# Performance work log

Hardware: AMD Instinct MI355X
Metric: run time of the kernel (lower is better)

## Reference

```python
import jax, jax.numpy as jnp
import numpy as np

NUM_WIRES = 18
N_LAYERS = 3
BATCH = 128
DIM = 2 ** NUM_WIRES


def setup_inputs() -> dict:
    key = jax.random.key(0)
    k1, k2, k3, k4, k5 = jax.random.split(key, 5)
    sr = jax.random.normal(k1, (BATCH, DIM), jnp.float32)
    si = jax.random.normal(k2, (BATCH, DIM), jnp.float32)
    norm = jnp.sqrt(jnp.sum(sr * sr + si * si, axis=1, keepdims=True))
    sr = sr / norm
    si = si / norm
    params = jax.random.normal(k3, (N_LAYERS, NUM_WIRES, 3), jnp.float32)
    head_w = jax.random.normal(k4, (1, NUM_WIRES), jnp.float32) * 0.1
    head_b = jax.random.normal(k5, (1,), jnp.float32) * 0.1
    return {"state_real": sr, "state_imag": si, "params": params,
            "head_w": head_w, "head_b": head_b}


def _gate_u(p):
    """Fused 2x2 unitary U = RZ(p2) @ RY(p1) @ RX(p0) (RX applied first)."""
    x, y, z = p[0], p[1], p[2]
    cx = jnp.cos(x / 2).astype(jnp.complex64)
    sx = jnp.sin(x / 2).astype(jnp.complex64)
    cy = jnp.cos(y / 2).astype(jnp.complex64)
    sy = jnp.sin(y / 2).astype(jnp.complex64)
    zero = jnp.zeros((), jnp.complex64)
    RX = jnp.stack([jnp.stack([cx, -1j * sx]), jnp.stack([-1j * sx, cx])])
    RY = jnp.stack([jnp.stack([cy, -sy]), jnp.stack([sy, cy])])
    ez = jnp.exp(-0.5j * z.astype(jnp.complex64))  # e^{-i z/2}
    RZ = jnp.stack([jnp.stack([ez, zero]), jnp.stack([zero, jnp.conj(ez)])])
    return RZ @ RY @ RX


def _apply_1q(state, U, w):
    # wire 0 = most significant bit (PennyLane default.qubit convention)
    b = state.shape[0]
    A = 2 ** w
    B = DIM // (2 * A)
    s = state.reshape(b, A, 2, B)
    s = jnp.einsum('ij,bajc->baic', U, s)
    return s.reshape(b, DIM)


def _apply_cz(state, w):
    b = state.shape[0]
    A = 2 ** w
    B = DIM // (4 * A)
    s = state.reshape(b, A, 2, 2, B)
    s = s.at[:, :, 1, 1, :].multiply(-1.0)
    return s.reshape(b, DIM)


def reference(state_real, state_imag, params, head_w, head_b):
    state = (state_real + 1j * state_imag).astype(jnp.complex64)
    for l in range(N_LAYERS):
        for w in range(NUM_WIRES):
            state = _apply_1q(state, _gate_u(params[l, w]), w)
        for w in range(NUM_WIRES - 1):
            state = _apply_cz(state, w)
    probs = state.real ** 2 + state.imag ** 2  # (B, DIM)
    feats = []
    for w in range(NUM_WIRES):
        A = 2 ** w
        B = DIM // (2 * A)
        p = probs.reshape(-1, A, 2, B).sum(axis=(1, 3))  # (batch, 2)
        feats.append(p[:, 0] - p[:, 1])  # <Z_w>
    feats = jnp.stack(feats, axis=1)  # (batch, num_wires)
    return (feats @ head_w.T + head_b)[:, 0]
```

## Files before the change

kernel.cpp:

```cpp
#include <hip/hip_runtime.h>

#define DBITS 18

typedef float v2f __attribute__((ext_vector_type(2)));

__device__ __forceinline__ int physx(int j){ return j ^ ((j>>4)&15) ^ ((j>>8)&15) ^ ((j>>12)&1); }

template<int b0,int b1,int b2,int b3>
__device__ __forceinline__ int dep4(int c){
  return ((c&1)<<b0) | (((c>>1)&1)<<b1) | (((c>>2)&1)<<b2) | (((c>>3)&1)<<b3);
}
template<int b0,int b1,int b2,int b3>
__device__ __forceinline__ int pdep4(int c){
  const int d = dep4<b0,b1,b2,b3>(c);
  return d ^ ((d>>4)&15) ^ ((d>>8)&15) ^ ((d>>12)&1);
}

__device__ __forceinline__ unsigned pack_bf2(v2f v){
  unsigned ur = __float_as_uint(v.x), ui = __float_as_uint(v.y);
  ur = (ur + 0x7FFFu + ((ur >> 16) & 1u)) >> 16;
  ui = (ui + 0x7FFFu + ((ui >> 16) & 1u)) & 0xFFFF0000u;
  return ur | ui;
}
__device__ __forceinline__ v2f unpack_bf2(unsigned u){
  v2f v; v.x = __uint_as_float(u << 16); v.y = __uint_as_float(u & 0xFFFF0000u); return v;
}

__device__ __forceinline__ v2f pk_mul(v2f x, v2f s){
  v2f r; asm("v_pk_mul_f32 %0, %1, %2" : "=v"(r) : "v"(x), "v"(s)); return r;
}
__device__ __forceinline__ v2f pk_mul_neg(v2f x, v2f s){
  v2f r; asm("v_pk_mul_f32 %0, %1, %2 neg_lo:[1,0] neg_hi:[1,0]" : "=v"(r) : "v"(x), "v"(s)); return r;
}
__device__ __forceinline__ v2f pk_fma(v2f x, v2f s, v2f a){
  v2f r; asm("v_pk_fma_f32 %0, %1, %2, %3" : "=v"(r) : "v"(x), "v"(s), "v"(a)); return r;
}
__device__ __forceinline__ v2f pk_fma_swlo(v2f x, v2f s, v2f a){
  v2f r; asm("v_pk_fma_f32 %0, %1, %2, %3 op_sel:[1,0,0] op_sel_hi:[0,1,1] neg_lo:[1,0,0]"
             : "=v"(r) : "v"(x), "v"(s), "v"(a)); return r;
}
__device__ __forceinline__ v2f pk_fma_swhi(v2f x, v2f s, v2f a){
  v2f r; asm("v_pk_fma_f32 %0, %1, %2, %3 op_sel:[1,0,0] op_sel_hi:[0,1,1] neg_hi:[1,0,0]"
             : "=v"(r) : "v"(x), "v"(s), "v"(a)); return r;
}

template<int S>
__device__ __forceinline__ void gate_pk(v2f a[16], const float* __restrict__ g){
  const v2f Ar = {g[0],g[0]}, Ai = {g[1],g[1]}, Br = {g[2],g[2]}, Bi = {g[3],g[3]};
  #pragma unroll
  for (int h = 0; h < 8; ++h){
    const int c0 = ((h & ~(S-1)) << 1) | (h & (S-1));
    const int c1 = c0 | S;
    const v2f X0 = a[c0], X1 = a[c1];
    v2f y0 = pk_mul(X0, Ar);
    y0 = pk_fma_swlo(X0, Ai, y0);
    y0 = pk_fma(X1, Br, y0);
    y0 = pk_fma_swlo(X1, Bi, y0);
    v2f y1 = pk_mul_neg(X0, Br);
    y1 = pk_fma_swlo(X0, Bi, y1);
    y1 = pk_fma(X1, Ar, y1);
    y1 = pk_fma_swhi(X1, Ai, y1);
    a[c0] = y0; a[c1] = y1;
  }
}

template<int CTRL>
__device__ __forceinline__ float dppf(float v){
  return __int_as_float(__builtin_amdgcn_update_dpp(0, __float_as_int(v), CTRL, 0xF, 0xF, true));
}
template<int CTRL>
__device__ __forceinline__ void gate_lane_pk(v2f a[16], const float* __restrict__ g, float s){
  const float uei = s*g[1], uor = s*g[2];
  const v2f UER = {g[0],g[0]}, UEI = {uei,uei}, UOR = {uor,uor}, UOI = {g[3],g[3]};
  #pragma unroll
  for (int c = 0; c < 16; ++c){
    const v2f X = a[c];
    v2f P; P.x = dppf<CTRL>(X.x); P.y = dppf<CTRL>(X.y);
    v2f y = pk_mul(X, UER);
    y = pk_fma_swlo(X, UEI, y);
    y = pk_fma(P, UOR, y);
    y = pk_fma_swlo(P, UOI, y);
    a[c] = y;
  }
}

__device__ __forceinline__ const float* gp(const float* __restrict__ gates, int L, int ggbit){
  return gates + (L*18 + (17 - ggbit))*4;
}
__device__ __forceinline__ void sgn(v2f& v, unsigned gg){
  const unsigned sb = (unsigned)(__popc(gg & (gg >> 1)) & 1) << 31;
  v.x = __uint_as_float(__float_as_uint(v.x) ^ sb);
  v.y = __uint_as_float(__float_as_uint(v.y) ^ sb);
}

template<int PASS>
__global__ __launch_bounds__(512, 4)
void qpass(const float* __restrict__ sr, const float* __restrict__ si,
           unsigned* __restrict__ st, const float* __restrict__ gates,
           const float* __restrict__ head_w, float* __restrict__ partials,
           int batch0)
{
  __shared__ v2f lds[8192];
  const int t = threadIdx.x;
  const int f  = (int)blockIdx.x & 31;
  const int bl = (int)blockIdx.x >> 5;
  const int bg = batch0 + bl;
  const unsigned stBase = ((unsigned)bl) << DBITS;
  const size_t  inBase  = ((size_t)bg) << DBITS;
  const float s1 = (t & 1) ? -1.f : 1.f;
  const float s2 = (t & 2) ? -1.f : 1.f;

  v2f a[16];

  if (PASS == 1){
    {
      const size_t base = inBase + ((size_t)f << 13) + (size_t)t;
      #pragma unroll
      for (int c = 0; c < 16; ++c){
        const size_t g = base + ((size_t)c << 9);
        a[c].x = sr[g]; a[c].y = si[g];
      }
      gate_pk<1>(a, gp(gates,0,9));
      gate_pk<2>(a, gp(gates,0,10));
      gate_pk<4>(a, gp(gates,0,11));
      gate_pk<8>(a, gp(gates,0,12));
      gate_lane_pk<0xB1>(a, gp(gates,0,0), s1);
      gate_lane_pk<0x4E>(a, gp(gates,0,1), s2);
      const int pj = physx(t);
      #pragma unroll
      for (int c = 0; c < 16; ++c) lds[pj ^ pdep4<9,10,11,12>(c)] = a[c];
    }
    __syncthreads();
    {
      const int jb = ((t&1)<<6)|(((t>>1)&1)<<7)|(((t>>2)&1)<<0)|(((t>>3)&1)<<1)|((t>>4)<<8);
      const int pj = physx(jb);
      #pragma unroll
      for (int c = 0; c < 16; ++c) a[c] = lds[pj ^ pdep4<2,3,4,5>(c)];
      gate_pk<1>(a, gp(gates,0,2));
      gate_pk<2>(a, gp(gates,0,3));
      gate_pk<4>(a, gp(gates,0,4));
      gate_pk<8>(a, gp(gates,0,5));
      gate_lane_pk<0xB1>(a, gp(gates,0,6), s1);
      gate_lane_pk<0x4E>(a, gp(gates,0,7), s2);
      #pragma unroll
      for (int c = 0; c < 16; ++c) lds[pj ^ pdep4<2,3,4,5>(c)] = a[c];
    }
    __syncthreads();
    {
      const int jb = (t&63)|(((t>>6)&1)<<6)|(((t>>7)&1)<<7)|(((t>>8)&1)<<12);
      const int pj = physx(jb);
      #pragma unroll
      for (int c = 0; c < 16; ++c) a[c] = lds[pj ^ pdep4<8,9,10,11>(c)];
      gate_pk<1>(a, gp(gates,0,8));
      const unsigned gb = (unsigned)(jb | (f << 13)) + stBase;
      #pragma unroll
      for (int c = 0; c < 16; ++c) st[gb + (unsigned)dep4<8,9,10,11>(c)] = pack_bf2(a[c]);
    }
  }
  else if (PASS == 2){
    {
      const unsigned gb = stBase + (unsigned)((t&255) | (((t>>8)&1)<<13) | (f<<8));
      #pragma unroll
      for (int c = 0; c < 16; ++c) a[c] = unpack_bf2(st[gb + ((unsigned)c<<14)]);
      gate_pk<1>(a, gp(gates,0,14));
      gate_pk<2>(a, gp(gates,0,15));
      gate_pk<4>(a, gp(gates,0,16));
      gate_pk<8>(a, gp(gates,0,17));
      const int pj = physx(t);
      #pragma unroll
      for (int c = 0; c < 16; ++c) lds[pj ^ pdep4<9,10,11,12>(c)] = a[c];
    }
    __syncthreads();
    {
      const int jb = ((t&1)<<10)|(((t>>1)&1)<<11)|(((t>>2)&1)<<0)|(((t>>3)&1)<<1)
                   | (((t>>4)&1)<<5)|(((t>>5)&1)<<6)|(((t>>6)&1)<<7)|(((t>>7)&1)<<9)|(((t>>8)&1)<<12);
      const int pj = physx(jb);
      #pragma unroll
      for (int c = 0; c < 16; ++c) a[c] = lds[pj ^ pdep4<8,2,3,4>(c)];
      gate_pk<1>(a, gp(gates,0,13));
      const unsigned gsb = (unsigned)((jb&255) | ((jb>>8)<<13) | (f<<8));
      #pragma unroll
      for (int c = 0; c < 16; ++c)
        sgn(a[c], gsb | (unsigned)(((c&1)<<13)|(((c>>1)&1)<<2)|(((c>>2)&1)<<3)|(((c>>3)&1)<<4)));
      gate_pk<1>(a, gp(gates,1,13));
      gate_pk<2>(a, gp(gates,1,2));
      gate_pk<4>(a, gp(gates,1,3));
      gate_pk<8>(a, gp(gates,1,4));
      gate_lane_pk<0xB1>(a, gp(gates,1,15), s1);
      gate_lane_pk<0x4E>(a, gp(gates,1,16), s2);
      #pragma unroll
      for (int c = 0; c < 16; ++c) lds[pj ^ pdep4<8,2,3,4>(c)] = a[c];
    }
    __syncthreads();
    {
      const int jb = (t&63)|(((t>>6)&1)<<8)|(((t>>7)&1)<<10)|(((t>>8)&1)<<11);
      const int pj = physx(jb);
      #pragma unroll
      for (int c = 0; c < 16; ++c) a[c] = lds[pj ^ pdep4<6,7,9,12>(c)];
      gate_pk<1>(a, gp(gates,1,6));
      gate_pk<2>(a, gp(gates,1,7));
      gate_pk<4>(a, gp(gates,1,14));
      gate_pk<8>(a, gp(gates,1,17));
      gate_lane_pk<0xB1>(a, gp(gates,1,0), s1);
      gate_lane_pk<0x4E>(a, gp(gates,1,1), s2);
      #pragma unroll
      for (int c = 0; c < 16; ++c){
        const int j = jb | dep4<6,7,9,12>(c);
        st[stBase + (unsigned)((j&255) | ((j>>8)<<13) | (f<<8))] = pack_bf2(a[c]);
      }
    }
  }
  else if (PASS == 3){
    const unsigned fp3 = (unsigned)(((f&3)<<6) | (((f>>2)&7)<<14));
    {
      const unsigned gb = stBase + (unsigned)((t&63) | (((t>>6)&7)<<8)) + fp3;
      #pragma unroll
      for (int c = 0; c < 16; ++c)
        a[c] = unpack_bf2(st[gb + (unsigned)(((c&7)<<11) | (((c>>3)&1)<<17))]);
      gate_pk<1>(a, gp(gates,1,11));
      gate_pk<2>(a, gp(gates,1,12));
      const int pj = physx(t);
      #pragma unroll
      for (int c = 0; c < 16; ++c) lds[pj ^ pdep4<9,10,11,12>(c)] = a[c];
    }
    __syncthreads();
    {
      const int jb = ((t&1)<<11)|(((t>>1)&1)<<12)|(((t>>2)&1)<<1)|(((t>>3)&1)<<2)
                   | (((t>>4)&1)<<0)|(((t>>5)&1)<<3)|(((t>>6)&1)<<4)|(((t>>7)&1)<<9)|(((t>>8)&1)<<10);
      const int pj = physx(jb);
      #pragma unroll
      for (int c = 0; c < 16; ++c) a[c] = lds[pj ^ pdep4<5,6,7,8>(c)];
      gate_pk<1>(a, gp(gates,1,5));
      gate_pk<2>(a, gp(gates,1,8));
      gate_pk<4>(a, gp(gates,1,9));
      gate_pk<8>(a, gp(gates,1,10));
      const unsigned gsb = (unsigned)((jb&63) | (((jb>>6)&63)<<8) | (((jb>>12)&1)<<17)) | fp3;
      #pragma unroll
      for (int c = 0; c < 16; ++c)
        sgn(a[c], gsb | (unsigned)(((c&1)<<5)|(((c>>1)&1)<<8)|(((c>>2)&1)<<9)|(((c>>3)&1)<<10)));
      gate_pk<1>(a, gp(gates,2,5));
      gate_pk<2>(a, gp(gates,2,8));
      gate_pk<4>(a, gp(gates,2,9));
      gate_pk<8>(a, gp(gates,2,10));
      gate_lane_pk<0xB1>(a, gp(gates,2,13), s1);
      gate_lane_pk<0x4E>(a, gp(gates,2,17), s2);
      #pragma unroll
      for (int c = 0; c < 16; ++c) lds[pj ^ pdep4<5,6,7,8>(c)] = a[c];
    }
    __syncthreads();
    {
      const int jb = (t&63)|(((t>>6)&1)<<6)|(((t>>7)&1)<<7)|(((t>>8)&1)<<12);
      const int pj = physx(jb);
      #pragma unroll
      for (int c = 0; c < 16; ++c) a[c] = lds[pj ^ pdep4<9,10,8,11>(c)];
      gate_pk<1>(a, gp(gates,2,11));
      gate_pk<2>(a, gp(gates,2,12));
      gate_lane_pk<0xB1>(a, gp(gates,2,0), s1);
      gate_lane_pk<0x4E>(a, gp(gates,2,1), s2);
      #pragma unroll
      for (int c = 0; c < 16; ++c){
        const int j = jb | dep4<9,10,8,11>(c);
        st[stBase + ((unsigned)((j&63) | (((j>>6)&63)<<8) | (((j>>12)&1)<<17)) | fp3)] = pack_bf2(a[c]);
      }
    }
  }
  else {
    const unsigned fp4 = (unsigned)(((f&15)<<10) | (((f>>4)&1)<<17));
    {
      const unsigned gb = stBase + (unsigned)t + fp4;
      #pragma unroll
      for (int c = 0; c < 16; ++c)
        a[c] = unpack_bf2(st[gb + (unsigned)(((c&1)<<9) | (((c>>1)&7)<<14))]);
      gate_pk<2>(a, gp(gates,2,14));
      gate_pk<4>(a, gp(gates,2,15));
      gate_pk<8>(a, gp(gates,2,16));
      const int pj = physx(t);
      #pragma unroll
      for (int c = 0; c < 16; ++c) lds[pj ^ pdep4<9,10,11,12>(c)] = a[c];
    }
    __syncthreads();
    {
      const int jb = ((t&1)<<7)|(((t>>1)&1)<<5)|(((t>>2)&1)<<0)|(((t>>3)&1)<<10)
                   | (((t>>4)&1)<<1)|(((t>>5)&1)<<8)|(((t>>6)&1)<<9)|(((t>>7)&1)<<11)|(((t>>8)&1)<<12);
      const int pj = physx(jb);
      #pragma unroll
      for (int c = 0; c < 16; ++c) a[c] = lds[pj ^ pdep4<2,3,4,6>(c)];
      gate_pk<1>(a, gp(gates,2,2));
      gate_pk<2>(a, gp(gates,2,3));
      gate_pk<4>(a, gp(gates,2,4));
      gate_pk<8>(a, gp(gates,2,6));
      gate_lane_pk<0xB1>(a, gp(gates,2,7), s1);
      const unsigned gg0 = (unsigned)((jb&1023) | (((jb>>10)&7)<<14)) | fp4;
      float cb = 0.f;
      #pragma unroll
      for (int k = 0; k < 18; ++k){
        const float hw = head_w[17-k];
        cb += ((gg0 >> k) & 1) ? -hw : hw;
      }
      const float d0 = -2.f*head_w[15], d1 = -2.f*head_w[14];
      const float d2 = -2.f*head_w[13], d3 = -2.f*head_w[11];
      float acc = 0.f;
      #pragma unroll
      for (int c = 0; c < 16; ++c){
        float coef = cb;
        if (c & 1) coef += d0;
        if (c & 2) coef += d1;
        if (c & 4) coef += d2;
        if (c & 8) coef += d3;
        acc += coef * (a[c].x*a[c].x + a[c].y*a[c].y);
      }
      __syncthreads();
      #pragma unroll
      for (int off = 32; off; off >>= 1) acc += __shfl_down(acc, off);
      float* red = reinterpret_cast<float*>(lds);
      if ((t & 63) == 0) red[t >> 6] = acc;
      __syncthreads();
      if (t == 0){
        float s = 0.f;
        #pragma unroll
        for (int i = 0; i < 8; ++i) s += red[i];
        partials[bg * 32 + f] = s;
      }
    }
  }
}

__global__ void qprep(const float* __restrict__ params, float* __restrict__ gates){
  const int tid = threadIdx.x;
  if (tid < 54){
    const float xx = params[tid*3+0]*0.5f, yy = params[tid*3+1]*0.5f, zz = params[tid*3+2]*0.5f;
    float sx,cx,sy,cy,sz,cz;
    sincosf(xx,&sx,&cx); sincosf(yy,&sy,&cy); sincosf(zz,&sz,&cz);
    float* g = gates + tid*4;
    g[0] =  cz*cy*cx + sz*sy*sx;
    g[1] =  cz*sy*sx - sz*cy*cx;
    g[2] = -cz*sy*cx - sz*cy*sx;
    g[3] =  sz*sy*cx - cz*cy*sx;
  }
}

__global__ void qfinal(const float* __restrict__ partials, const float* __restrict__ head_b,
                       float* __restrict__ out, int B){
  const int b = threadIdx.x + blockIdx.x * blockDim.x;
  if (b < B){
    float s = head_b[0];
    #pragma unroll
    for (int i = 0; i < 32; ++i) s += partials[b*32 + i];
    out[b] = s;
  }
}

extern "C" void kernel_launch(void* const* d_in, const int* in_sizes, int n_in,
                              void* d_out, int out_size, void* d_ws, size_t ws_size,
                              hipStream_t stream){
  const float* sr     = (const float*)d_in[0];
  const float* si     = (const float*)d_in[1];
  const float* params = (const float*)d_in[2];
  const float* head_w = (const float*)d_in[3];
  const float* head_b = (const float*)d_in[4];
  float* out = (float*)d_out;
  const int B = in_sizes[0] >> DBITS;

  float*    gates    = (float*)d_ws;
  float*    partials = (float*)((char*)d_ws + 4096);
  unsigned* st       = (unsigned*)((char*)d_ws + 24576);

  size_t stBytes = ws_size > 24576 ? ws_size - 24576 : 0;
  int maxChunk = (int)(stBytes / ((size_t)(1 << DBITS) * 4));
  if (maxChunk > B) maxChunk = B;
  if (maxChunk < 1) maxChunk = 1;

  qprep<<<dim3(1), dim3(64), 0, stream>>>(params, gates);

  for (int b0 = 0; b0 < B; b0 += maxChunk){
    const int c = (B - b0 < maxChunk) ? (B - b0) : maxChunk;
    dim3 grid(c * 32), blk(512);
    qpass<1><<<grid, blk, 0, stream>>>(sr, si, st, gates, head_w, partials, b0);
    qpass<2><<<grid, blk, 0, stream>>>(sr, si, st, gates, head_w, partials, b0);
    qpass<3><<<grid, blk, 0, stream>>>(sr, si, st, gates, head_w, partials, b0);
    qpass<4><<<grid, blk, 0, stream>>>(sr, si, st, gates, head_w, partials, b0);
  }
  qfinal<<<dim3(1), dim3(128), 0, stream>>>(partials, head_b, out, B);
}
```

Baseline: 395.3 us.

## Repartition passes to 1024-thread blocks with 8 amplitudes per thread and XCD-aware block remap

Restructures all four state-vector passes so each 1024-thread block holds an 8192-amplitude tile, with 8 amplitudes per thread instead of 16. The wire-to-pass assignment, LDS swizzle and global access patterns are redesigned: the first pass uses float4 loads, later passes fuse more gates and CZ sign flips per pass, and the last pass no longer needs an LDS exchange. A block-index remap spreads consecutive logical tiles across the 8 XCDs for L2 locality. This aims to cut register pressure and raise occupancy and memory coalescing, at the cost of bigger blocks, new swizzle logic and more warps per reduction.

After: 401.3 us. Within noise of the previous version (+1.5%).

```diff
diff --git a/kernel.cpp b/kernel.cpp
--- a/kernel.cpp
+++ b/kernel.cpp
@@ -4,17 +4,16 @@
 
 typedef float v2f __attribute__((ext_vector_type(2)));
 
-__device__ __forceinline__ int physx(int j){ return j ^ ((j>>4)&15) ^ ((j>>8)&15) ^ ((j>>12)&1); }
-
-template<int b0,int b1,int b2,int b3>
-__device__ __forceinline__ int dep4(int c){
-  return ((c&1)<<b0) | (((c>>1)&1)<<b1) | (((c>>2)&1)<<b2) | (((c>>3)&1)<<b3);
-}
-template<int b0,int b1,int b2,int b3>
-__device__ __forceinline__ int pdep4(int c){
-  const int d = dep4<b0,b1,b2,b3>(c);
-  return d ^ ((d>>4)&15) ^ ((d>>8)&15) ^ ((d>>12)&1);
-}
+__device__ __forceinline__ constexpr int physb(int j){
+  return j ^ (((j>>4)&1)<<1) ^ (((j>>5)&1)<<2) ^ (((j>>6)&1)<<3) ^ (((j>>6)&1)<<0)
+           ^ (((j>>8)&1)<<2) ^ (((j>>9)&1)<<3);
+}
+template<int b0,int b1,int b2>
+__device__ __forceinline__ int dep3(int c){
+  return ((c&1)<<b0) | (((c>>1)&1)<<b1) | (((c>>2)&1)<<b2);
+}
+template<int b0,int b1,int b2>
+__device__ __forceinline__ int pb3(int c){ return physb(dep3<b0,b1,b2>(c)); }
 
 __device__ __forceinline__ unsigned pack_bf2(v2f v){
   unsigned ur = __float_as_uint(v.x), ui = __float_as_uint(v.y);
@@ -45,10 +44,10 @@
 }
 
 template<int S>
-__device__ __forceinline__ void gate_pk(v2f a[16], const float* __restrict__ g){
+__device__ __forceinline__ void gate_pk8(v2f a[8], const float* __restrict__ g){
   const v2f Ar = {g[0],g[0]}, Ai = {g[1],g[1]}, Br = {g[2],g[2]}, Bi = {g[3],g[3]};
   #pragma unroll
-  for (int h = 0; h < 8; ++h){
+  for (int h = 0; h < 4; ++h){
     const int c0 = ((h & ~(S-1)) << 1) | (h & (S-1));
     const int c1 = c0 | S;
     const v2f X0 = a[c0], X1 = a[c1];
@@ -69,11 +68,11 @@
   return __int_as_float(__builtin_amdgcn_update_dpp(0, __float_as_int(v), CTRL, 0xF, 0xF, true));
 }
 template<int CTRL>
-__device__ __forceinline__ void gate_lane_pk(v2f a[16], const float* __restrict__ g, float s){
+__device__ __forceinline__ void gate_lane8(v2f a[8], const float* __restrict__ g, float s){
   const float uei = s*g[1], uor = s*g[2];
   const v2f UER = {g[0],g[0]}, UEI = {uei,uei}, UOR = {uor,uor}, UOI = {g[3],g[3]};
   #pragma unroll
-  for (int c = 0; c < 16; ++c){
+  for (int c = 0; c < 8; ++c){
     const v2f X = a[c];
     v2f P; P.x = dppf<CTRL>(X.x); P.y = dppf<CTRL>(X.y);
     v2f y = pk_mul(X, UER);
@@ -94,7 +93,7 @@
 }
 
 template<int PASS>
-__global__ __launch_bounds__(512, 4)
+__global__ __launch_bounds__(1024, 8)
 void qpass(const float* __restrict__ sr, const float* __restrict__ si,
            unsigned* __restrict__ st, const float* __restrict__ gates,
            const float* __restrict__ head_w, float* __restrict__ partials,
@@ -102,214 +101,203 @@
 {
   __shared__ v2f lds[8192];
   const int t = threadIdx.x;
-  const int f  = (int)blockIdx.x & 31;
-  const int bl = (int)blockIdx.x >> 5;
+
+  const int nwg = (int)gridDim.x;
+  const int p = (int)blockIdx.x;
+  const int q = nwg >> 3, r = nwg & 7, x = p & 7, m = p >> 3;
+  const int logical = (x < r ? x*(q+1) : r*(q+1) + (x-r)*q) + m;
+  const int f  = logical & 31;
+  const int bl = logical >> 5;
   const int bg = batch0 + bl;
   const unsigned stBase = ((unsigned)bl) << DBITS;
   const size_t  inBase  = ((size_t)bg) << DBITS;
   const float s1 = (t & 1) ? -1.f : 1.f;
   const float s2 = (t & 2) ? -1.f : 1.f;
 
-  v2f a[16];
+  v2f a[8];
 
   if (PASS == 1){
     {
-      const size_t base = inBase + ((size_t)f << 13) + (size_t)t;
-      #pragma unroll
-      for (int c = 0; c < 16; ++c){
-        const size_t g = base + ((size_t)c << 9);
-        a[c].x = sr[g]; a[c].y = si[g];
-      }
-      gate_pk<1>(a, gp(gates,0,9));
-      gate_pk<2>(a, gp(gates,0,10));
-      gate_pk<4>(a, gp(gates,0,11));
-      gate_pk<8>(a, gp(gates,0,12));
-      gate_lane_pk<0xB1>(a, gp(gates,0,0), s1);
-      gate_lane_pk<0x4E>(a, gp(gates,0,1), s2);
-      const int pj = physx(t);
-      #pragma unroll
-      for (int c = 0; c < 16; ++c) lds[pj ^ pdep4<9,10,11,12>(c)] = a[c];
-    }
-    __syncthreads();
-    {
-      const int jb = ((t&1)<<6)|(((t>>1)&1)<<7)|(((t>>2)&1)<<0)|(((t>>3)&1)<<1)|((t>>4)<<8);
-      const int pj = physx(jb);
-      #pragma unroll
-      for (int c = 0; c < 16; ++c) a[c] = lds[pj ^ pdep4<2,3,4,5>(c)];
-      gate_pk<1>(a, gp(gates,0,2));
-      gate_pk<2>(a, gp(gates,0,3));
-      gate_pk<4>(a, gp(gates,0,4));
-      gate_pk<8>(a, gp(gates,0,5));
-      gate_lane_pk<0xB1>(a, gp(gates,0,6), s1);
-      gate_lane_pk<0x4E>(a, gp(gates,0,7), s2);
-      #pragma unroll
-      for (int c = 0; c < 16; ++c) lds[pj ^ pdep4<2,3,4,5>(c)] = a[c];
-    }
-    __syncthreads();
-    {
-      const int jb = (t&63)|(((t>>6)&1)<<6)|(((t>>7)&1)<<7)|(((t>>8)&1)<<12);
-      const int pj = physx(jb);
-      #pragma unroll
-      for (int c = 0; c < 16; ++c) a[c] = lds[pj ^ pdep4<8,9,10,11>(c)];
-      gate_pk<1>(a, gp(gates,0,8));
-      const unsigned gb = (unsigned)(jb | (f << 13)) + stBase;
-      #pragma unroll
-      for (int c = 0; c < 16; ++c) st[gb + (unsigned)dep4<8,9,10,11>(c)] = pack_bf2(a[c]);
+      const int jb = ((t&1)<<3) | (((t>>1)&1)<<4) | ((t>>2)<<5);
+      const size_t base = inBase + ((size_t)f << 13) + (size_t)jb;
+      const float4 r0 = *(const float4*)(sr+base);
+      const float4 r1 = *(const float4*)(sr+base+4);
+      const float4 i0 = *(const float4*)(si+base);
+      const float4 i1 = *(const float4*)(si+base+4);
+      a[0] = {r0.x,i0.x}; a[1] = {r0.y,i0.y}; a[2] = {r0.z,i0.z}; a[3] = {r0.w,i0.w};
+      a[4] = {r1.x,i1.x}; a[5] = {r1.y,i1.y}; a[6] = {r1.z,i1.z}; a[7] = {r1.w,i1.w};
+      gate_pk8<1>(a, gp(gates,0,0));
+      gate_pk8<2>(a, gp(gates,0,1));
+      gate_pk8<4>(a, gp(gates,0,2));
+      gate_lane8<0xB1>(a, gp(gates,0,3), s1);
+      gate_lane8<0x4E>(a, gp(gates,0,4), s2);
+      const int pj = physb(jb);
+      #pragma unroll
+      for (int c = 0; c < 8; ++c) lds[pj ^ pb3<0,1,2>(c)] = a[c];
+    }
+    __syncthreads();
+    {
+      const int jb = ((t&1)<<8)|(((t>>1)&1)<<9)|(((t>>2)&1)<<0)|(((t>>3)&1)<<1)
+                   | (((t>>4)&1)<<2)|(((t>>5)&1)<<3)|(((t>>6)&1)<<4)
+                   | (((t>>7)&1)<<10)|(((t>>8)&1)<<11)|(((t>>9)&1)<<12);
+      const int pj = physb(jb);
+      #pragma unroll
+      for (int c = 0; c < 8; ++c) a[c] = lds[pj ^ pb3<5,6,7>(c)];
+      gate_pk8<1>(a, gp(gates,0,5));
+      gate_pk8<2>(a, gp(gates,0,6));
+      gate_pk8<4>(a, gp(gates,0,7));
+      gate_lane8<0xB1>(a, gp(gates,0,8), s1);
+      gate_lane8<0x4E>(a, gp(gates,0,9), s2);
+      #pragma unroll
+      for (int c = 0; c < 8; ++c) lds[pj ^ pb3<5,6,7>(c)] = a[c];
+    }
+    __syncthreads();
+    {
+      const int pj = physb(t);
+      #pragma unroll
+      for (int c = 0; c < 8; ++c) a[c] = lds[pj ^ pb3<10,11,12>(c)];
+      gate_pk8<1>(a, gp(gates,0,10));
+      gate_pk8<2>(a, gp(gates,0,11));
+      gate_pk8<4>(a, gp(gates,0,12));
+      const unsigned gb = stBase + (unsigned)((f<<13) | t);
+      #pragma unroll
+      for (int c = 0; c < 8; ++c) st[gb + ((unsigned)c<<10)] = pack_bf2(a[c]);
     }
   }
   else if (PASS == 2){
     {
-      const unsigned gb = stBase + (unsigned)((t&255) | (((t>>8)&1)<<13) | (f<<8));
-      #pragma unroll
-      for (int c = 0; c < 16; ++c) a[c] = unpack_bf2(st[gb + ((unsigned)c<<14)]);
-      gate_pk<1>(a, gp(gates,0,14));
-      gate_pk<2>(a, gp(gates,0,15));
-      gate_pk<4>(a, gp(gates,0,16));
-      gate_pk<8>(a, gp(gates,0,17));
-      const int pj = physx(t);
-      #pragma unroll
-      for (int c = 0; c < 16; ++c) lds[pj ^ pdep4<9,10,11,12>(c)] = a[c];
-    }
-    __syncthreads();
-    {
-      const int jb = ((t&1)<<10)|(((t>>1)&1)<<11)|(((t>>2)&1)<<0)|(((t>>3)&1)<<1)
-                   | (((t>>4)&1)<<5)|(((t>>5)&1)<<6)|(((t>>6)&1)<<7)|(((t>>7)&1)<<9)|(((t>>8)&1)<<12);
-      const int pj = physx(jb);
-      #pragma unroll
-      for (int c = 0; c < 16; ++c) a[c] = lds[pj ^ pdep4<8,2,3,4>(c)];
-      gate_pk<1>(a, gp(gates,0,13));
-      const unsigned gsb = (unsigned)((jb&255) | ((jb>>8)<<13) | (f<<8));
-      #pragma unroll
-      for (int c = 0; c < 16; ++c)
-        sgn(a[c], gsb | (unsigned)(((c&1)<<13)|(((c>>1)&1)<<2)|(((c>>2)&1)<<3)|(((c>>3)&1)<<4)));
-      gate_pk<1>(a, gp(gates,1,13));
-      gate_pk<2>(a, gp(gates,1,2));
-      gate_pk<4>(a, gp(gates,1,3));
-      gate_pk<8>(a, gp(gates,1,4));
-      gate_lane_pk<0xB1>(a, gp(gates,1,15), s1);
-      gate_lane_pk<0x4E>(a, gp(gates,1,16), s2);
-      #pragma unroll
-      for (int c = 0; c < 16; ++c) lds[pj ^ pdep4<8,2,3,4>(c)] = a[c];
-    }
-    __syncthreads();
-    {
-      const int jb = (t&63)|(((t>>6)&1)<<8)|(((t>>7)&1)<<10)|(((t>>8)&1)<<11);
-      const int pj = physx(jb);
-      #pragma unroll
-      for (int c = 0; c < 16; ++c) a[c] = lds[pj ^ pdep4<6,7,9,12>(c)];
-      gate_pk<1>(a, gp(gates,1,6));
-      gate_pk<2>(a, gp(gates,1,7));
-      gate_pk<4>(a, gp(gates,1,14));
-      gate_pk<8>(a, gp(gates,1,17));
-      gate_lane_pk<0xB1>(a, gp(gates,1,0), s1);
-      gate_lane_pk<0x4E>(a, gp(gates,1,1), s2);
-      #pragma unroll
-      for (int c = 0; c < 16; ++c){
-        const int j = jb | dep4<6,7,9,12>(c);
+      const int jb = ((t&1)<<8)|(((t>>1)&1)<<9)|((t>>2)&255);
+      const unsigned gg0 = (unsigned)((jb&255) | ((jb>>8)<<13) | (f<<8));
+      const unsigned gb = stBase + gg0;
+      #pragma unroll
+      for (int c = 0; c < 8; ++c) a[c] = unpack_bf2(st[gb + ((unsigned)c<<15)]);
+      gate_pk8<1>(a, gp(gates,0,15));
+      gate_pk8<2>(a, gp(gates,0,16));
+      gate_pk8<4>(a, gp(gates,0,17));
+      gate_lane8<0xB1>(a, gp(gates,0,13), s1);
+      gate_lane8<0x4E>(a, gp(gates,0,14), s2);
+      #pragma unroll
+      for (int c = 0; c < 8; ++c) sgn(a[c], gg0 + ((unsigned)c<<15));
+      gate_pk8<1>(a, gp(gates,1,15));
+      gate_pk8<2>(a, gp(gates,1,16));
+      gate_pk8<4>(a, gp(gates,1,17));
+      gate_lane8<0xB1>(a, gp(gates,1,13), s1);
+      gate_lane8<0x4E>(a, gp(gates,1,14), s2);
+      const int pj = physb(jb);
+      #pragma unroll
+      for (int c = 0; c < 8; ++c) lds[pj ^ pb3<10,11,12>(c)] = a[c];
+    }
+    __syncthreads();
+    {
+      const int jb = ((t&1)<<3) | (((t>>1)&1)<<4) | ((t>>2)<<5);
+      const int pj = physb(jb);
+      #pragma unroll
+      for (int c = 0; c < 8; ++c) a[c] = lds[pj ^ pb3<0,1,2>(c)];
+      gate_pk8<1>(a, gp(gates,1,0));
+      gate_pk8<2>(a, gp(gates,1,1));
+      gate_pk8<4>(a, gp(gates,1,2));
+      gate_lane8<0xB1>(a, gp(gates,1,3), s1);
+      gate_lane8<0x4E>(a, gp(gates,1,4), s2);
+      #pragma unroll
+      for (int c = 0; c < 8; ++c) lds[pj ^ pb3<0,1,2>(c)] = a[c];
+    }
+    __syncthreads();
+    {
+      const int jb = (t&31) | (((t>>5)&31)<<8);
+      const int pj = physb(jb);
+      #pragma unroll
+      for (int c = 0; c < 8; ++c) a[c] = lds[pj ^ pb3<5,6,7>(c)];
+      gate_pk8<1>(a, gp(gates,1,5));
+      gate_pk8<2>(a, gp(gates,1,6));
+      gate_pk8<4>(a, gp(gates,1,7));
+      #pragma unroll
+      for (int c = 0; c < 8; ++c){
+        const int j = jb | dep3<5,6,7>(c);
         st[stBase + (unsigned)((j&255) | ((j>>8)<<13) | (f<<8))] = pack_bf2(a[c]);
       }
     }
   }
   else if (PASS == 3){
-    const unsigned fp3 = (unsigned)(((f&3)<<6) | (((f>>2)&7)<<14));
-    {
-      const unsigned gb = stBase + (unsigned)((t&63) | (((t>>6)&7)<<8)) + fp3;
-      #pragma unroll
-      for (int c = 0; c < 16; ++c)
-        a[c] = unpack_bf2(st[gb + (unsigned)(((c&7)<<11) | (((c>>3)&1)<<17))]);
-      gate_pk<1>(a, gp(gates,1,11));
-      gate_pk<2>(a, gp(gates,1,12));
-      const int pj = physx(t);
-      #pragma unroll
-      for (int c = 0; c < 16; ++c) lds[pj ^ pdep4<9,10,11,12>(c)] = a[c];
-    }
-    __syncthreads();
-    {
-      const int jb = ((t&1)<<11)|(((t>>1)&1)<<12)|(((t>>2)&1)<<1)|(((t>>3)&1)<<2)
-                   | (((t>>4)&1)<<0)|(((t>>5)&1)<<3)|(((t>>6)&1)<<4)|(((t>>7)&1)<<9)|(((t>>8)&1)<<10);
-      const int pj = physx(jb);
-      #pragma unroll
-      for (int c = 0; c < 16; ++c) a[c] = lds[pj ^ pdep4<5,6,7,8>(c)];
-      gate_pk<1>(a, gp(gates,1,5));
-      gate_pk<2>(a, gp(gates,1,8));
-      gate_pk<4>(a, gp(gates,1,9));
-      gate_pk<8>(a, gp(gates,1,10));
-      const unsigned gsb = (unsigned)((jb&63) | (((jb>>6)&63)<<8) | (((jb>>12)&1)<<17)) | fp3;
-      #pragma unroll
-      for (int c = 0; c < 16; ++c)
-        sgn(a[c], gsb | (unsigned)(((c&1)<<5)|(((c>>1)&1)<<8)|(((c>>2)&1)<<9)|(((c>>3)&1)<<10)));
-      gate_pk<1>(a, gp(gates,2,5));
-      gate_pk<2>(a, gp(gates,2,8));
-      gate_pk<4>(a, gp(gates,2,9));
-      gate_pk<8>(a, gp(gates,2,10));
-      gate_lane_pk<0xB1>(a, gp(gates,2,13), s1);
-      gate_lane_pk<0x4E>(a, gp(gates,2,17), s2);
-      #pragma unroll
-      for (int c = 0; c < 16; ++c) lds[pj ^ pdep4<5,6,7,8>(c)] = a[c];
-    }
-    __syncthreads();
-    {
-      const int jb = (t&63)|(((t>>6)&1)<<6)|(((t>>7)&1)<<7)|(((t>>8)&1)<<12);
-      const int pj = physx(jb);
-      #pragma unroll
-      for (int c = 0; c < 16; ++c) a[c] = lds[pj ^ pdep4<9,10,8,11>(c)];
-      gate_pk<1>(a, gp(gates,2,11));
-      gate_pk<2>(a, gp(gates,2,12));
-      gate_lane_pk<0xB1>(a, gp(gates,2,0), s1);
-      gate_lane_pk<0x4E>(a, gp(gates,2,1), s2);
-      #pragma unroll
-      for (int c = 0; c < 16; ++c){
-        const int j = jb | dep4<9,10,8,11>(c);
-        st[stBase + ((unsigned)((j&63) | (((j>>6)&63)<<8) | (((j>>12)&1)<<17)) | fp3)] = pack_bf2(a[c]);
+    {
+      const int jb = ((t&1)<<8)|(((t>>1)&1)<<9)|((t>>2)&255);
+      const unsigned gg0 = (unsigned)(jb | (f<<13));
+      const unsigned gb = stBase + gg0;
+      #pragma unroll
+      for (int c = 0; c < 8; ++c) a[c] = unpack_bf2(st[gb + ((unsigned)c<<10)]);
+      gate_pk8<1>(a, gp(gates,1,10));
+      gate_pk8<2>(a, gp(gates,1,11));
+      gate_pk8<4>(a, gp(gates,1,12));
+      gate_lane8<0xB1>(a, gp(gates,1,8), s1);
+      gate_lane8<0x4E>(a, gp(gates,1,9), s2);
+      #pragma unroll
+      for (int c = 0; c < 8; ++c) sgn(a[c], gg0 + ((unsigned)c<<10));
+      gate_pk8<1>(a, gp(gates,2,10));
+      gate_pk8<2>(a, gp(gates,2,11));
+      gate_pk8<4>(a, gp(gates,2,12));
+      gate_lane8<0xB1>(a, gp(gates,2,8), s1);
+      gate_lane8<0x4E>(a, gp(gates,2,9), s2);
+      const int pj = physb(jb);
+      #pragma unroll
+      for (int c = 0; c < 8; ++c) lds[pj ^ pb3<10,11,12>(c)] = a[c];
+    }
+    __syncthreads();
+    {
+      const int jb = (t&3) | ((t>>2)<<5);
+      const int pj = physb(jb);
+      #pragma unroll
+      for (int c = 0; c < 8; ++c) a[c] = lds[pj ^ pb3<2,3,4>(c)];
+      gate_pk8<1>(a, gp(gates,2,2));
+      gate_pk8<2>(a, gp(gates,2,3));
+      gate_pk8<4>(a, gp(gates,2,4));
+      gate_lane8<0xB1>(a, gp(gates,2,0), s1);
+      gate_lane8<0x4E>(a, gp(gates,2,1), s2);
+      #pragma unroll
+      for (int c = 0; c < 8; ++c) lds[pj ^ pb3<2,3,4>(c)] = a[c];
+    }
+    __syncthreads();
+    {
+      const int jb = (t&31) | (((t>>5)&31)<<8);
+      const int pj = physb(jb);
+      #pragma unroll
+      for (int c = 0; c < 8; ++c) a[c] = lds[pj ^ pb3<5,6,7>(c)];
+      gate_pk8<1>(a, gp(gates,2,5));
+      gate_pk8<2>(a, gp(gates,2,6));
+      gate_pk8<4>(a, gp(gates,2,7));
+      #pragma unroll
+      for (int c = 0; c < 8; ++c){
+        const int j = jb | dep3<5,6,7>(c);
+        st[stBase + (unsigned)(j | (f<<13))] = pack_bf2(a[c]);
       }
     }
   }
   else {
-    const unsigned fp4 = (unsigned)(((f&15)<<10) | (((f>>4)&1)<<17));
-    {
-      const unsigned gb = stBase + (unsigned)t + fp4;
-      #pragma unroll
-      for (int c = 0; c < 16; ++c)
-        a[c] = unpack_bf2(st[gb + (unsigned)(((c&1)<<9) | (((c>>1)&7)<<14))]);
-      gate_pk<2>(a, gp(gates,2,14));
-      gate_pk<4>(a, gp(gates,2,15));
-      gate_pk<8>(a, gp(gates,2,16));
-      const int pj = physx(t);
-      #pragma unroll
-      for (int c = 0; c < 16; ++c) lds[pj ^ pdep4<9,10,11,12>(c)] = a[c];
-    }
-    __syncthreads();
-    {
-      const int jb = ((t&1)<<7)|(((t>>1)&1)<<5)|(((t>>2)&1)<<0)|(((t>>3)&1)<<10)
-                   | (((t>>4)&1)<<1)|(((t>>5)&1)<<8)|(((t>>6)&1)<<9)|(((t>>7)&1)<<11)|(((t>>8)&1)<<12);
-      const int pj = physx(jb);
-      #pragma unroll
-      for (int c = 0; c < 16; ++c) a[c] = lds[pj ^ pdep4<2,3,4,6>(c)];
-      gate_pk<1>(a, gp(gates,2,2));
-      gate_pk<2>(a, gp(gates,2,3));
-      gate_pk<4>(a, gp(gates,2,4));
-      gate_pk<8>(a, gp(gates,2,6));
-      gate_lane_pk<0xB1>(a, gp(gates,2,7), s1);
-      const unsigned gg0 = (unsigned)((jb&1023) | (((jb>>10)&7)<<14)) | fp4;
+    {
+      const int jb = ((t&1)<<8)|(((t>>1)&1)<<9)|((t>>2)&255);
+      const unsigned gg0 = (unsigned)((jb&255) | ((jb>>8)<<13) | (f<<8));
+      const unsigned gb = stBase + gg0;
+      #pragma unroll
+      for (int c = 0; c < 8; ++c) a[c] = unpack_bf2(st[gb + ((unsigned)c<<15)]);
+      gate_pk8<1>(a, gp(gates,2,15));
+      gate_pk8<2>(a, gp(gates,2,16));
+      gate_pk8<4>(a, gp(gates,2,17));
+      gate_lane8<0xB1>(a, gp(gates,2,13), s1);
+      gate_lane8<0x4E>(a, gp(gates,2,14), s2);
       float cb = 0.f;
       #pragma unroll
       for (int k = 0; k < 18; ++k){
         const float hw = head_w[17-k];
         cb += ((gg0 >> k) & 1) ? -hw : hw;
       }
-      const float d0 = -2.f*head_w[15], d1 = -2.f*head_w[14];
-      const float d2 = -2.f*head_w[13], d3 = -2.f*head_w[11];
+      const float d0 = -2.f*head_w[2], d1 = -2.f*head_w[1], d2 = -2.f*head_w[0];
       float acc = 0.f;
       #pragma unroll
-      for (int c = 0; c < 16; ++c){
+      for (int c = 0; c < 8; ++c){
         float coef = cb;
         if (c & 1) coef += d0;
         if (c & 2) coef += d1;
         if (c & 4) coef += d2;
-        if (c & 8) coef += d3;
         acc += coef * (a[c].x*a[c].x + a[c].y*a[c].y);
       }
-      __syncthreads();
       #pragma unroll
       for (int off = 32; off; off >>= 1) acc += __shfl_down(acc, off);
       float* red = reinterpret_cast<float*>(lds);
@@ -318,7 +306,7 @@
       if (t == 0){
         float s = 0.f;
         #pragma unroll
-        for (int i = 0; i < 8; ++i) s += red[i];
+        for (int i = 0; i < 16; ++i) s += red[i];
         partials[bg * 32 + f] = s;
       }
     }
@@ -374,7 +362,7 @@
 
   for (int b0 = 0; b0 < B; b0 += maxChunk){
     const int c = (B - b0 < maxChunk) ? (B - b0) : maxChunk;
-    dim3 grid(c * 32), blk(512);
+    dim3 grid(c * 32), blk(1024);
     qpass<1><<<grid, blk, 0, stream>>>(sr, si, st, gates, head_w, partials, b0);
     qpass<2><<<grid, blk, 0, stream>>>(sr, si, st, gates, head_w, partials, b0);
     qpass<3><<<grid, blk, 0, stream>>>(sr, si, st, gates, head_w, partials, b0);
```
